# Optimization experiments

Hardware: AMD Instinct MI355X
Metric: run time of the kernel (lower is better)

Reference implementation:

```python
import jax, jax.numpy as jnp
import numpy as np

# Stickbreaking attention (IBM ModuleFormer style) as in the torch module:
#   logits = q @ k^T / sqrt(head_dim)  (causal)
#   z = sigmoid(logits), log_beta = logsigmoid(-logits), both causally masked
#   re_cum_log_beta = einsum('bhij,jk->bhik', log_beta, tril(ones(S,S)))
#     -> re[i,k] = sum_{k <= j <= i} log_beta[i, j]   (full tril incl. diagonal,
#        exactly as written in the source: cum_weight = torch.tril(torch.ones(L,L)))
#   weights = z * exp(re_cum_log_beta);  out = weights @ v
# Note: the torch code applies the causal mask by adding -inf; the only finite,
# NaN-free expression of that math (matching ModuleFormer's masked_fill) is to
# zero out masked entries of z and log_beta before the triangular matmul.

B, H, S, D = 2, 16, 1024, 64


def setup_inputs() -> dict:
    key = jax.random.key(0)
    kq, kk, kv = jax.random.split(key, 3)
    q = jax.random.normal(kq, (B, H, S, D), dtype=jnp.float32)
    k = jax.random.normal(kk, (B, H, S, D), dtype=jnp.float32)
    v = jax.random.normal(kv, (B, H, S, D), dtype=jnp.float32)
    return {"q": q, "k": k, "v": v}


def reference(q, k, v):
    head_dim = q.shape[-1]
    scaling = 1.0 / np.sqrt(head_dim).astype(np.float32)
    # [B,H,S,S] attention logits
    logits = jnp.einsum("bhqd,bhkd->bhqk", q, k) * scaling
    seq = logits.shape[-1]
    causal = jnp.tril(jnp.ones((seq, seq), dtype=logits.dtype))  # 1 where j<=i
    z = jax.nn.sigmoid(logits) * causal
    log_beta = jax.nn.log_sigmoid(-logits) * causal
    cum_weight = jnp.tril(jnp.ones((seq, seq), dtype=logits.dtype))
    # re[i,k] = sum_{j>=k} log_beta[i,j] (log_beta already 0 for j>i)
    re_cum_log_beta = jnp.einsum("bhij,jk->bhik", log_beta, cum_weight)
    weights = z * jnp.exp(re_cum_log_beta)
    return jnp.einsum("bhqk,bhkd->bhqd", weights, v)
```

## Files before the change

### kernel.cpp

```cpp
#include <hip/hip_runtime.h>
#include <hip/hip_bf16.h>
#include <math.h>


typedef __attribute__((ext_vector_type(8))) short short8;
typedef __attribute__((ext_vector_type(4))) short short4v;
typedef __attribute__((ext_vector_type(4))) float f32x4;

#define PITCH 72

__device__ inline short bf16r(float x) {
    __hip_bfloat16 h = __float2bfloat16(x);
    return *(short*)&h;
}
__device__ inline float bf16f(short s) {
    union { unsigned u; float f; } c;
    c.u = ((unsigned)(unsigned short)s) << 16;
    return c.f;
}

__global__ __launch_bounds__(256, 2) void stickbreak_mfma(
    const float* __restrict__ Qg, const float* __restrict__ Kg,
    const float* __restrict__ Vg, float* __restrict__ Og)
{
    __shared__ __align__(16) short Kh[64 * PITCH];
    __shared__ __align__(16) short Kl[64 * PITCH];
    __shared__ __align__(16) short Vt[64 * PITCH];
    __shared__ __align__(16) short Ws[64 * PITCH];

    const int t = threadIdx.x;
    const int n = blockIdx.x;
    const int bh = (n & 7) + 8 * (n >> 7);
    const int qr = (n >> 3) & 15;
    const int qt = (n >> 8) ? (15 - qr) : qr;

    const size_t hbase = (size_t)bh * 1024 * 64;
    const float* qp = Qg + hbase + (size_t)qt * 64 * 64;
    const float* kp = Kg + hbase;
    const float* vp = Vg + hbase;
    float*       op = Og + hbase + (size_t)qt * 64 * 64;

    const int lane = t & 63;
    const int wv   = t >> 6;
    const int l16  = lane & 15;
    const int q4   = lane >> 4;

    const int srow = t >> 2;
    const int scol = (t & 3) << 4;
    const int vj   = (t & 15) << 2;
    const int vd   = (t >> 4) << 2;

    short8 qfh[2], qfl[2];
    {
        const float* qrow = qp + (16 * wv + l16) * 64;
        #pragma unroll
        for (int ks = 0; ks < 2; ++ks) {
            const int base = 32 * ks + 8 * q4;
            const float4 f0 = *(const float4*)(qrow + base);
            const float4 f1 = *(const float4*)(qrow + base + 4);
            float a[8] = {f0.x, f0.y, f0.z, f0.w, f1.x, f1.y, f1.z, f1.w};
            #pragma unroll
            for (int j = 0; j < 8; ++j) {
                const short hi = bf16r(a[j]);
                qfh[ks][j] = hi;
                qfl[ks][j] = bf16r(a[j] - bf16f(hi));
            }
        }
    }

    f32x4 Oacc[4];
    #pragma unroll
    for (int i = 0; i < 4; ++i) Oacc[i] = (f32x4){0.f, 0.f, 0.f, 0.f};
    float Crow = 0.f;

    float4 kreg[4], vreg[4];
    {
        const float* ksrc = kp + (size_t)qt * 4096 + srow * 64 + scol;
        const float* vsrc = vp + (size_t)qt * 4096;
        #pragma unroll
        for (int i = 0; i < 4; ++i) kreg[i] = *(const float4*)(ksrc + 4 * i);
        #pragma unroll
        for (int r = 0; r < 4; ++r) vreg[r] = *(const float4*)(vsrc + (vj + r) * 64 + vd);
    }

    for (int kt = qt; kt >= 0; --kt) {
        {
            short8 h0, h1, l0, l1;
            #pragma unroll
            for (int i = 0; i < 4; ++i) {
                float a[4] = {kreg[i].x, kreg[i].y, kreg[i].z, kreg[i].w};
                #pragma unroll
                for (int j = 0; j < 4; ++j) {
                    const short hi = bf16r(a[j]);
                    const short lo = bf16r(a[j] - bf16f(hi));
                    const int idx = 4 * i + j;
                    if (idx < 8) { h0[idx] = hi; l0[idx] = lo; }
                    else         { h1[idx - 8] = hi; l1[idx - 8] = lo; }
                }
            }
            *(short8*)&Kh[srow * PITCH + scol]     = h0;
            *(short8*)&Kh[srow * PITCH + scol + 8] = h1;
            *(short8*)&Kl[srow * PITCH + scol]     = l0;
            *(short8*)&Kl[srow * PITCH + scol + 8] = l1;
        }
        {
            #pragma unroll
            for (int x = 0; x < 4; ++x) {
                float rr[4] = { x == 0 ? vreg[0].x : x == 1 ? vreg[0].y : x == 2 ? vreg[0].z : vreg[0].w,
                                x == 0 ? vreg[1].x : x == 1 ? vreg[1].y : x == 2 ? vreg[1].z : vreg[1].w,
                                x == 0 ? vreg[2].x : x == 1 ? vreg[2].y : x == 2 ? vreg[2].z : vreg[2].w,
                                x == 0 ? vreg[3].x : x == 1 ? vreg[3].y : x == 2 ? vreg[3].z : vreg[3].w };
                short4v w4;
                #pragma unroll
                for (int r = 0; r < 4; ++r) w4[r] = bf16r(rr[r]);
                *(short4v*)&Vt[(vd + x) * PITCH + vj] = w4;
            }
        }
        __syncthreads();

        if (kt > 0) {
            const float* ksrc = kp + (size_t)(kt - 1) * 4096 + srow * 64 + scol;
            const float* vsrc = vp + (size_t)(kt - 1) * 4096;
            #pragma unroll
            for (int i = 0; i < 4; ++i) kreg[i] = *(const float4*)(ksrc + 4 * i);
            #pragma unroll
            for (int r = 0; r < 4; ++r) vreg[r] = *(const float4*)(vsrc + (vj + r) * 64 + vd);
        }

        f32x4 Sacc[4];
        #pragma unroll
        for (int i = 0; i < 4; ++i) Sacc[i] = (f32x4){0.f, 0.f, 0.f, 0.f};
        #pragma unroll
        for (int ks = 0; ks < 2; ++ks) {
            #pragma unroll
            for (int nt = 0; nt < 4; ++nt) {
                const short8 ah = *(const short8*)&Kh[(16 * nt + l16) * PITCH + 32 * ks + 8 * q4];
                const short8 al = *(const short8*)&Kl[(16 * nt + l16) * PITCH + 32 * ks + 8 * q4];
                Sacc[nt] = __builtin_amdgcn_mfma_f32_16x16x32_bf16(ah, qfh[ks], Sacc[nt], 0, 0, 0);
                Sacc[nt] = __builtin_amdgcn_mfma_f32_16x16x32_bf16(al, qfh[ks], Sacc[nt], 0, 0, 0);
                Sacc[nt] = __builtin_amdgcn_mfma_f32_16x16x32_bf16(ah, qfl[ks], Sacc[nt], 0, 0, 0);
            }
        }

        const bool diag = (kt == qt);
        const int irow = 16 * wv + l16;
        float ex[4][4];
        float sR[4];
        #pragma unroll
        for (int nt = 0; nt < 4; ++nt) {
            float lbr[4], lv[4];
            #pragma unroll
            for (int reg = 0; reg < 4; ++reg) {
                float l = Sacc[nt][reg] * 0.125f;
                if (diag && (16 * nt + 4 * q4 + reg > irow)) l = -1e30f;
                const float e  = __expf(-fabsf(l));
                const float lb = -(fmaxf(l, 0.f) + __logf(1.f + e));
                lv[reg] = l; lbr[reg] = lb;
            }
            const float s3 = lbr[3];
            const float s2 = lbr[2] + s3;
            const float s1 = lbr[1] + s2;
            const float s0 = lbr[0] + s1;
            ex[nt][0] = lv[0] + lbr[0] + s0;
            ex[nt][1] = lv[1] + lbr[1] + s1;
            ex[nt][2] = lv[2] + lbr[2] + s2;
            ex[nt][3] = lv[3] + lbr[3] + s3;
            sR[nt] = s0;
        }
        float gq[4], Tn[4];
        #pragma unroll
        for (int nt = 0; nt < 4; ++nt) {
            float g = sR[nt];
            float u = __shfl_down(g, 16, 64); if (q4 < 3) g += u;
            u = __shfl_down(g, 32, 64);       if (q4 < 2) g += u;
            gq[nt] = g;
            Tn[nt] = __shfl(g, l16, 64);
        }
        const float TSa[4] = { Tn[1] + Tn[2] + Tn[3], Tn[2] + Tn[3], Tn[3], 0.f };
        #pragma unroll
        for (int nt = 0; nt < 4; ++nt) {
            const float cross = (gq[nt] - sR[nt]) + TSa[nt] + Crow;
            short4v w4;
            #pragma unroll
            for (int reg = 0; reg < 4; ++reg)
                w4[reg] = bf16r(__expf(ex[nt][reg] + cross));
            *(short4v*)&Ws[irow * PITCH + 16 * nt + 4 * q4] = w4;
        }
        Crow += TSa[0] + Tn[0];

        __syncthreads();

        #pragma unroll
        for (int ks = 0; ks < 2; ++ks) {
            const short8 wa = *(const short8*)&Ws[(16 * wv + l16) * PITCH + 32 * ks + 8 * q4];
            #pragma unroll
            for (int dt = 0; dt < 4; ++dt) {
                const short8 vb = *(const short8*)&Vt[(16 * dt + l16) * PITCH + 32 * ks + 8 * q4];
                Oacc[dt] = __builtin_amdgcn_mfma_f32_16x16x32_bf16(wa, vb, Oacc[dt], 0, 0, 0);
            }
        }

        __syncthreads();
    }

    #pragma unroll
    for (int dt = 0; dt < 4; ++dt)
        #pragma unroll
        for (int r = 0; r < 4; ++r)
            op[(16 * wv + 4 * q4 + r) * 64 + 16 * dt + l16] = Oacc[dt][r];
}

extern "C" void kernel_launch(void* const* d_in, const int* in_sizes, int n_in,
                              void* d_out, int out_size, void* d_ws, size_t ws_size,
                              hipStream_t stream) {
    const float* q = (const float*)d_in[0];
    const float* k = (const float*)d_in[1];
    const float* v = (const float*)d_in[2];
    float* out = (float*)d_out;
    stickbreak_mfma<<<dim3(512), dim3(256), 0, stream>>>(q, k, v, out);
}
```

Measured before the change: 106.5 us.

## Double-buffer K/V tiles in LDS and cut per-iteration barriers to one

K-hi/lo and transposed V tiles now live in two LDS buffers. The next tile is converted and stored into the alternate buffer after the PV matmul, and global loads run two tiles ahead in registers. The barrier between the weight-tile write and the PV matmul is dropped, since each wave reads only its own Ws rows, and the remaining barrier is a custom lgkmcnt wait plus s_barrier. The goal is fewer block-wide syncs and better overlap of global latency with compute. The cost is more LDS per block, roughly 64.5KB, which puts pressure on the 2-blocks-per-CU target.

```diff
diff --git a/kernel.cpp b/kernel.cpp
--- a/kernel.cpp
+++ b/kernel.cpp
@@ -19,13 +19,20 @@
     return c.f;
 }
 
+__device__ inline void lds_barrier() {
+    __builtin_amdgcn_sched_barrier(0);
+    asm volatile("s_waitcnt lgkmcnt(0)" ::: "memory");
+    __builtin_amdgcn_s_barrier();
+    __builtin_amdgcn_sched_barrier(0);
+}
+
 __global__ __launch_bounds__(256, 2) void stickbreak_mfma(
     const float* __restrict__ Qg, const float* __restrict__ Kg,
     const float* __restrict__ Vg, float* __restrict__ Og)
 {
-    __shared__ __align__(16) short Kh[64 * PITCH];
-    __shared__ __align__(16) short Kl[64 * PITCH];
-    __shared__ __align__(16) short Vt[64 * PITCH];
+    __shared__ __align__(16) short Kh[2][64 * PITCH];
+    __shared__ __align__(16) short Kl[2][64 * PITCH];
+    __shared__ __align__(16) short Vt[2][64 * PITCH];
     __shared__ __align__(16) short Ws[64 * PITCH];
 
     const int t = threadIdx.x;
@@ -74,58 +81,54 @@
     float Crow = 0.f;
 
     float4 kreg[4], vreg[4];
-    {
-        const float* ksrc = kp + (size_t)qt * 4096 + srow * 64 + scol;
-        const float* vsrc = vp + (size_t)qt * 4096;
+
+    auto prefetch_tile = [&](int tt) {
+        const float* ksrc = kp + (size_t)tt * 4096 + srow * 64 + scol;
+        const float* vsrc = vp + (size_t)tt * 4096;
         #pragma unroll
         for (int i = 0; i < 4; ++i) kreg[i] = *(const float4*)(ksrc + 4 * i);
         #pragma unroll
         for (int r = 0; r < 4; ++r) vreg[r] = *(const float4*)(vsrc + (vj + r) * 64 + vd);
-    }
+    };
+
+    auto stage_tile = [&](int nb) {
+        short8 h0, h1, l0, l1;
+        #pragma unroll
+        for (int i = 0; i < 4; ++i) {
+            float a[4] = {kreg[i].x, kreg[i].y, kreg[i].z, kreg[i].w};
+            #pragma unroll
+            for (int j = 0; j < 4; ++j) {
+                const short hi = bf16r(a[j]);
+                const short lo = bf16r(a[j] - bf16f(hi));
+                const int idx = 4 * i + j;
+                if (idx < 8) { h0[idx] = hi; l0[idx] = lo; }
+                else         { h1[idx - 8] = hi; l1[idx - 8] = lo; }
+            }
+        }
+        *(short8*)&Kh[nb][srow * PITCH + scol]     = h0;
+        *(short8*)&Kh[nb][srow * PITCH + scol + 8] = h1;
+        *(short8*)&Kl[nb][srow * PITCH + scol]     = l0;
+        *(short8*)&Kl[nb][srow * PITCH + scol + 8] = l1;
+        #pragma unroll
+        for (int x = 0; x < 4; ++x) {
+            float rr[4] = { x == 0 ? vreg[0].x : x == 1 ? vreg[0].y : x == 2 ? vreg[0].z : vreg[0].w,
+                            x == 0 ? vreg[1].x : x == 1 ? vreg[1].y : x == 2 ? vreg[1].z : vreg[1].w,
+                            x == 0 ? vreg[2].x : x == 1 ? vreg[2].y : x == 2 ? vreg[2].z : vreg[2].w,
+                            x == 0 ? vreg[3].x : x == 1 ? vreg[3].y : x == 2 ? vreg[3].z : vreg[3].w };
+            short4v w4;
+            #pragma unroll
+            for (int r = 0; r < 4; ++r) w4[r] = bf16r(rr[r]);
+            *(short4v*)&Vt[nb][(vd + x) * PITCH + vj] = w4;
+        }
+    };
+
+    prefetch_tile(qt);
+    stage_tile(0);
+    if (qt > 0) prefetch_tile(qt - 1);
+    lds_barrier();
 
     for (int kt = qt; kt >= 0; --kt) {
-        {
-            short8 h0, h1, l0, l1;
-            #pragma unroll
-            for (int i = 0; i < 4; ++i) {
-                float a[4] = {kreg[i].x, kreg[i].y, kreg[i].z, kreg[i].w};
-                #pragma unroll
-                for (int j = 0; j < 4; ++j) {
-                    const short hi = bf16r(a[j]);
-                    const short lo = bf16r(a[j] - bf16f(hi));
-                    const int idx = 4 * i + j;
-                    if (idx < 8) { h0[idx] = hi; l0[idx] = lo; }
-                    else         { h1[idx - 8] = hi; l1[idx - 8] = lo; }
-                }
-            }
-            *(short8*)&Kh[srow * PITCH + scol]     = h0;
-            *(short8*)&Kh[srow * PITCH + scol + 8] = h1;
-            *(short8*)&Kl[srow * PITCH + scol]     = l0;
-            *(short8*)&Kl[srow * PITCH + scol + 8] = l1;
-        }
-        {
-            #pragma unroll
-            for (int x = 0; x < 4; ++x) {
-                float rr[4] = { x == 0 ? vreg[0].x : x == 1 ? vreg[0].y : x == 2 ? vreg[0].z : vreg[0].w,
-                                x == 0 ? vreg[1].x : x == 1 ? vreg[1].y : x == 2 ? vreg[1].z : vreg[1].w,
-                                x == 0 ? vreg[2].x : x == 1 ? vreg[2].y : x == 2 ? vreg[2].z : vreg[2].w,
-                                x == 0 ? vreg[3].x : x == 1 ? vreg[3].y : x == 2 ? vreg[3].z : vreg[3].w };
-                short4v w4;
-                #pragma unroll
-                for (int r = 0; r < 4; ++r) w4[r] = bf16r(rr[r]);
-                *(short4v*)&Vt[(vd + x) * PITCH + vj] = w4;
-            }
-        }
-        __syncthreads();
-
-        if (kt > 0) {
-            const float* ksrc = kp + (size_t)(kt - 1) * 4096 + srow * 64 + scol;
-            const float* vsrc = vp + (size_t)(kt - 1) * 4096;
-            #pragma unroll
-            for (int i = 0; i < 4; ++i) kreg[i] = *(const float4*)(ksrc + 4 * i);
-            #pragma unroll
-            for (int r = 0; r < 4; ++r) vreg[r] = *(const float4*)(vsrc + (vj + r) * 64 + vd);
-        }
+        const int cur = (qt - kt) & 1;
 
         f32x4 Sacc[4];
         #pragma unroll
@@ -134,8 +137,8 @@
         for (int ks = 0; ks < 2; ++ks) {
             #pragma unroll
             for (int nt = 0; nt < 4; ++nt) {
-                const short8 ah = *(const short8*)&Kh[(16 * nt + l16) * PITCH + 32 * ks + 8 * q4];
-                const short8 al = *(const short8*)&Kl[(16 * nt + l16) * PITCH + 32 * ks + 8 * q4];
+                const short8 ah = *(const short8*)&Kh[cur][(16 * nt + l16) * PITCH + 32 * ks + 8 * q4];
+                const short8 al = *(const short8*)&Kl[cur][(16 * nt + l16) * PITCH + 32 * ks + 8 * q4];
                 Sacc[nt] = __builtin_amdgcn_mfma_f32_16x16x32_bf16(ah, qfh[ks], Sacc[nt], 0, 0, 0);
                 Sacc[nt] = __builtin_amdgcn_mfma_f32_16x16x32_bf16(al, qfh[ks], Sacc[nt], 0, 0, 0);
                 Sacc[nt] = __builtin_amdgcn_mfma_f32_16x16x32_bf16(ah, qfl[ks], Sacc[nt], 0, 0, 0);
@@ -188,19 +191,21 @@
         }
         Crow += TSa[0] + Tn[0];
 
-        __syncthreads();
-
         #pragma unroll
         for (int ks = 0; ks < 2; ++ks) {
             const short8 wa = *(const short8*)&Ws[(16 * wv + l16) * PITCH + 32 * ks + 8 * q4];
             #pragma unroll
             for (int dt = 0; dt < 4; ++dt) {
-                const short8 vb = *(const short8*)&Vt[(16 * dt + l16) * PITCH + 32 * ks + 8 * q4];
+                const short8 vb = *(const short8*)&Vt[cur][(16 * dt + l16) * PITCH + 32 * ks + 8 * q4];
                 Oacc[dt] = __builtin_amdgcn_mfma_f32_16x16x32_bf16(wa, vb, Oacc[dt], 0, 0, 0);
             }
         }
 
-        __syncthreads();
+        if (kt > 0) {
+            stage_tile(cur ^ 1);
+            if (kt > 1) prefetch_tile(kt - 2);
+            lds_barrier();
+        }
     }
 
     #pragma unroll
```

Measured after the change: 103.8 us. -2.6%, faster.
